# Optimization experiments

Hardware: AMD Instinct MI355X
Metric: run time of the kernel (lower is better)

The kernel has to match this reference:

```python
import jax, jax.numpy as jnp
import numpy as np

HIDDEN = 2048
N_HEADS = 16
HEAD_DIM = HIDDEN // N_HEADS
BATCH = 2
SEQ = 2048
N_CP = max(8, int(HIDDEN * HIDDEN / 128.9))  # 32540 control points


def _spline_to_weight(cp, out_dim, in_dim):
    # Reconstruct full weight matrix by sampling the control-point curve at
    # out_dim*in_dim evenly spaced parameter values (piecewise-linear spline eval).
    n = cp.shape[0]
    t = jnp.linspace(0.0, 1.0, out_dim * in_dim)
    xp = jnp.linspace(0.0, 1.0, n)
    return jnp.interp(t, xp, cp).reshape(out_dim, in_dim)


def setup_inputs() -> dict:
    key = jax.random.key(0)
    ks = jax.random.split(key, 5)
    hidden_states = jax.random.normal(ks[0], (BATCH, SEQ, HIDDEN), dtype=jnp.float32)
    cp_q = jax.random.normal(ks[1], (N_CP,), dtype=jnp.float32) * 0.02
    cp_k = jax.random.normal(ks[2], (N_CP,), dtype=jnp.float32) * 0.02
    cp_v = jax.random.normal(ks[3], (N_CP,), dtype=jnp.float32) * 0.02
    cp_o = jax.random.normal(ks[4], (N_CP,), dtype=jnp.float32) * 0.02
    # additive causal mask [1,1,S,S]
    causal = jnp.tril(jnp.ones((SEQ, SEQ), dtype=bool))
    attention_mask = jnp.where(causal, 0.0, -1e9).astype(jnp.float32)[None, None]
    return {
        'hidden_states': hidden_states,
        'cp_q': cp_q, 'cp_k': cp_k, 'cp_v': cp_v, 'cp_o': cp_o,
        'attention_mask': attention_mask,
    }


def reference(hidden_states, cp_q, cp_k, cp_v, cp_o, attention_mask):
    B, S, H = hidden_states.shape
    q_w = _spline_to_weight(cp_q, H, H)
    k_w = _spline_to_weight(cp_k, H, H)
    v_w = _spline_to_weight(cp_v, H, H)
    o_w = _spline_to_weight(cp_o, H, H)

    # F.linear(x, W) == x @ W.T
    q = (hidden_states @ q_w.T).reshape(B, S, N_HEADS, HEAD_DIM).transpose(0, 2, 1, 3)
    k = (hidden_states @ k_w.T).reshape(B, S, N_HEADS, HEAD_DIM).transpose(0, 2, 1, 3)
    v = (hidden_states @ v_w.T).reshape(B, S, N_HEADS, HEAD_DIM).transpose(0, 2, 1, 3)

    scale = 1.0 / np.sqrt(HEAD_DIM).astype(np.float32)
    scores = jnp.einsum('bhqd,bhkd->bhqk', q, k) * scale + attention_mask
    probs = jax.nn.softmax(scores.astype(jnp.float32), axis=-1).astype(q.dtype)
    attn = jnp.einsum('bhqk,bhkd->bhqd', probs, v)
    attn = attn.transpose(0, 2, 1, 3).reshape(B, S, H)
    return attn @ o_w.T
```

## Files before the change

### kernel.cpp

```cpp
#include <hip/hip_runtime.h>
#include <stdint.h>

typedef unsigned short u16;
typedef __bf16 bf16x8 __attribute__((ext_vector_type(8)));
typedef float f32x4 __attribute__((ext_vector_type(4)));
typedef u16 u16x4 __attribute__((ext_vector_type(4)));

#define MFMA16(a, b, c) __builtin_amdgcn_mfma_f32_16x16x32_bf16((a), (b), (c), 0, 0, 0)

__device__ __forceinline__ u16 f2bf(float f) {
  uint32_t u = __builtin_bit_cast(uint32_t, f);
  u += 0x7FFFu + ((u >> 16) & 1u);
  return (u16)(u >> 16);
}
__device__ __forceinline__ bf16x8 cvt8(f32x4 lo, f32x4 hi) {
  union { u16 u[8]; bf16x8 v; } r;
#pragma unroll
  for (int j = 0; j < 4; j++) { r.u[j] = f2bf(lo[j]); r.u[4 + j] = f2bf(hi[j]); }
  return r.v;
}
__device__ __forceinline__ void gld_lds16(const void* g, void* l) {
  __builtin_amdgcn_global_load_lds(
      (const __attribute__((address_space(1))) uint32_t*)g,
      (__attribute__((address_space(3))) uint32_t*)l, 16, 0, 0);
}

__global__ void prep_kernel(const float* __restrict__ x, const float* __restrict__ cpq,
                            const float* __restrict__ cpk, const float* __restrict__ cpv,
                            const float* __restrict__ cpo, u16* __restrict__ xb,
                            u16* __restrict__ Wqkv, u16* __restrict__ Wo,
                            int n, double factor) {
  int blk = blockIdx.x;
  if (blk < 65536) {
    int idx = blk * 256 + threadIdx.x;
    int w = idx >> 22;
    int i = idx & 4194303;
    const float* cp = (w == 0) ? cpq : (w == 1) ? cpk : (w == 2) ? cpv : cpo;
    double u = (double)i * factor;
    int i0 = (int)u;
    if (i0 > n - 2) i0 = n - 2;
    float fr = (float)(u - (double)i0);
    float f0 = cp[i0], f1 = cp[i0 + 1];
    u16 bv = f2bf(f0 + fr * (f1 - f0));
    if (w < 3) Wqkv[idx] = bv; else Wo[i] = bv;
  } else {
    size_t i = ((size_t)(blk - 65536) * 256 + threadIdx.x) * 8;
    const f32x4* p = (const f32x4*)(x + i);
    *(bf16x8*)(xb + i) = cvt8(p[0], p[1]);
  }
}

__global__ __launch_bounds__(512, 2)
void gemm_qkv(const u16* __restrict__ A, const u16* __restrict__ B,
              u16* __restrict__ oQ, u16* __restrict__ oK, u16* __restrict__ oV) {
  __shared__ __align__(16) u16 As[3 * 128 * 64];
  __shared__ __align__(16) u16 Bs[3 * 256 * 64];
  const int tid = threadIdx.x;
  const int wave = tid >> 6, lane = tid & 63, quad = lane >> 4, l16 = lane & 15;
  const int wm = wave & 1, wn = wave >> 1;

  const int m0 = blockIdx.y * 128, n0 = blockIdx.x * 256;

  size_t aoffg[2], boffg[4];
  int lA[2], lB[4];
#pragma unroll
  for (int u = 0; u < 2; u++) {
    int s = u * 512 + tid, r = s >> 3, c = s & 7, gc = c ^ (r & 7);
    lA[u] = s * 16;
    aoffg[u] = (size_t)(m0 + r) * 4096 + gc * 16;
  }
#pragma unroll
  for (int u = 0; u < 4; u++) {
    int s = u * 512 + tid, r = s >> 3, c = s & 7, gc = c ^ (r & 7);
    lB[u] = s * 16;
    boffg[u] = (size_t)(n0 + r) * 4096 + gc * 16;
  }

  int roA[4], roB[4];
#pragma unroll
  for (int mi = 0; mi < 4; mi++) {
    int row = wm * 64 + mi * 16 + l16;
    roA[mi] = row * 128 + ((quad ^ (row & 7)) * 16);
  }
#pragma unroll
  for (int nj = 0; nj < 4; nj++) {
    int row = wn * 64 + nj * 16 + l16;
    roB[nj] = row * 128 + ((quad ^ (row & 7)) * 16);
  }

  const char* Ab = (const char*)A;
  const char* Bb = (const char*)B;
  char* AsB = (char*)As;
  char* BsB = (char*)Bs;

  f32x4 acc[4][4];
  const f32x4 fz = {0.f, 0.f, 0.f, 0.f};
#pragma unroll
  for (int i = 0; i < 4; i++)
#pragma unroll
    for (int j = 0; j < 4; j++) acc[i][j] = fz;

#define QKV_STAGE(TT, NX)                                                     \
  do {                                                                        \
    size_t kb = (size_t)(TT) * 128;                                           \
    gld_lds16(Ab + aoffg[0] + kb, AsB + (NX) * 16384 + lA[0]);                \
    gld_lds16(Ab + aoffg[1] + kb, AsB + (NX) * 16384 + lA[1]);                \
    gld_lds16(Bb + boffg[0] + kb, BsB + (NX) * 32768 + lB[0]);                \
    gld_lds16(Bb + boffg[1] + kb, BsB + (NX) * 32768 + lB[1]);                \
    gld_lds16(Bb + boffg[2] + kb, BsB + (NX) * 32768 + lB[2]);                \
    gld_lds16(Bb + boffg[3] + kb, BsB + (NX) * 32768 + lB[3]);                \
  } while (0)

#define QKV_BODY(T, CUR, NX, STG, WM)                                         \
  do {                                                                        \
    if (STG) QKV_STAGE((T) + 2, NX);                                          \
    _Pragma("unroll") for (int t = 0; t < 2; t++) {                           \
      bf16x8 af[4], bfv[4];                                                   \
      _Pragma("unroll") for (int mi = 0; mi < 4; mi++)                        \
          af[mi] = *(const bf16x8*)(AsB + (CUR) * 16384 + (roA[mi] ^ (t * 64))); \
      _Pragma("unroll") for (int nj = 0; nj < 4; nj++)                        \
          bfv[nj] = *(const bf16x8*)(BsB + (CUR) * 32768 + (roB[nj] ^ (t * 64))); \
      __builtin_amdgcn_s_setprio(1);                                          \
      _Pragma("unroll") for (int mi = 0; mi < 4; mi++)                        \
          _Pragma("unroll") for (int nj = 0; nj < 4; nj++)                    \
              acc[mi][nj] = MFMA16(af[mi], bfv[nj], acc[mi][nj]);             \
      __builtin_amdgcn_s_setprio(0);                                          \
    }                                                                         \
    if ((WM) == 6) asm volatile("s_waitcnt vmcnt(6)" ::: "memory");           \
    else if ((WM) == 0) asm volatile("s_waitcnt vmcnt(0)" ::: "memory");      \
    if ((WM) >= 0) {                                                          \
      __builtin_amdgcn_s_barrier();                                           \
      __builtin_amdgcn_sched_barrier(0);                                      \
    }                                                                         \
  } while (0)

  QKV_STAGE(0, 0);
  QKV_STAGE(1, 1);
  asm volatile("s_waitcnt vmcnt(6)" ::: "memory");
  __builtin_amdgcn_s_barrier();
  __builtin_amdgcn_sched_barrier(0);

  for (int t = 0; t < 30; t += 3) {
    QKV_BODY(t, 0, 2, true, 6);
    QKV_BODY(t + 1, 1, 0, true, 6);
    QKV_BODY(t + 2, 2, 1, true, 6);
  }
  QKV_BODY(30, 0, 2, false, 0);
  QKV_BODY(31, 1, 0, false, -1);
#undef QKV_BODY
#undef QKV_STAGE

  const float qscale = 0.08838834764831845f;
#pragma unroll
  for (int j = 0; j < 4; j++) {
    int nb = n0 + wn * 64 + j * 16;
    int sel = nb >> 11;
    int h = (nb >> 7) & 15;
    int d = (nb & 127) + l16;
#pragma unroll
    for (int i = 0; i < 4; i++) {
      int mrow = m0 + wm * 64 + i * 16 + quad * 4;
      int bq = mrow >> 11, srow = mrow & 2047;
      if (sel == 2) {
        u16x4 pk = {f2bf(acc[i][j][0]), f2bf(acc[i][j][1]),
                    f2bf(acc[i][j][2]), f2bf(acc[i][j][3])};
        *(u16x4*)&oV[(size_t)(((bq << 4) + h) * 128 + d) * 2048 + srow] = pk;
      } else if (sel == 0) {
        int base = ((bq << 4) + h) * 2048;
#pragma unroll
        for (int r = 0; r < 4; r++)
          oQ[(size_t)(base + srow + r) * 128 + d] = f2bf(acc[i][j][r] * qscale);
      } else {
        int base = ((bq << 4) + h) * 2048;
#pragma unroll
        for (int r = 0; r < 4; r++)
          oK[(size_t)(base + srow + r) * 128 + d] = f2bf(acc[i][j][r]);
      }
    }
  }
}

template <int MODE>
__global__ __launch_bounds__(256, 2)
void gemm_bt(const u16* __restrict__ A, const u16* __restrict__ B,
             u16* __restrict__ oQ, u16* __restrict__ oK, u16* __restrict__ oV,
             float* __restrict__ oC) {
  constexpr int KD = 2048;
  __shared__ __align__(16) u16 As[128 * 64];
  __shared__ __align__(16) u16 Bs[128 * 64];
  const int tid = threadIdx.x;
  const int wave = tid >> 6, lane = tid & 63, quad = lane >> 4, l16 = lane & 15;
  const int wm = wave & 1, wn = wave >> 1;
  const int m0 = blockIdx.y * 128, n0 = blockIdx.x * 128;

  size_t aoff[4], boff[4];
  int lslot[4];
#pragma unroll
  for (int b = 0; b < 4; b++) {
    int s = wave * 256 + b * 64 + lane;
    int r = s >> 3, c = s & 7, gc = c ^ (r & 7);
    lslot[b] = s * 16;
    aoff[b] = (size_t)(m0 + r) * (KD * 2) + gc * 16;
    boff[b] = (size_t)(n0 + r) * (KD * 2) + gc * 16;
  }
  const char* Ab = (const char*)A;
  const char* Bb = (const char*)B;
  char* AsB = (char*)As;
  char* BsB = (char*)Bs;

  f32x4 acc[4][4];
  const f32x4 fz = {0.f, 0.f, 0.f, 0.f};
#pragma unroll
  for (int i = 0; i < 4; i++)
#pragma unroll
    for (int j = 0; j < 4; j++) acc[i][j] = fz;

  for (int kt = 0; kt < KD / 64; ++kt) {
    if (kt) __syncthreads();
#pragma unroll
    for (int b = 0; b < 4; b++) {
      gld_lds16(Ab + aoff[b], AsB + lslot[b]);
      gld_lds16(Bb + boff[b], BsB + lslot[b]);
      aoff[b] += 128;
      boff[b] += 128;
    }
    __syncthreads();
#pragma unroll
    for (int t = 0; t < 2; t++) {
      bf16x8 af[4], bfb[4];
#pragma unroll
      for (int i = 0; i < 4; i++) {
        int row = wm * 64 + i * 16 + l16;
        int ch = (t * 4 + quad) ^ (row & 7);
        af[i] = *(const bf16x8*)(AsB + row * 128 + ch * 16);
      }
#pragma unroll
      for (int j = 0; j < 4; j++) {
        int row = wn * 64 + j * 16 + l16;
        int ch = (t * 4 + quad) ^ (row & 7);
        bfb[j] = *(const bf16x8*)(BsB + row * 128 + ch * 16);
      }
#pragma unroll
      for (int i = 0; i < 4; i++)
#pragma unroll
        for (int j = 0; j < 4; j++) acc[i][j] = MFMA16(af[i], bfb[j], acc[i][j]);
    }
  }

  if (MODE == 0) {
    const float qscale = 0.08838834764831845f;
#pragma unroll
    for (int j = 0; j < 4; j++) {
      int nb = n0 + wn * 64 + j * 16;
      int sel = nb >> 11;
      int h = (nb >> 7) & 15;
      int d = (nb & 127) + l16;
#pragma unroll
      for (int i = 0; i < 4; i++) {
        int mrow = m0 + wm * 64 + i * 16 + quad * 4;
        int bq = mrow >> 11, srow = mrow & 2047;
        if (sel == 2) {
          u16x4 pk = {f2bf(acc[i][j][0]), f2bf(acc[i][j][1]),
                      f2bf(acc[i][j][2]), f2bf(acc[i][j][3])};
          *(u16x4*)&oV[(size_t)(((bq << 4) + h) * 128 + d) * 2048 + srow] = pk;
        } else if (sel == 0) {
          int base = ((bq << 4) + h) * 2048;
#pragma unroll
          for (int r = 0; r < 4; r++)
            oQ[(size_t)(base + srow + r) * 128 + d] = f2bf(acc[i][j][r] * qscale);
        } else {
          int base = ((bq << 4) + h) * 2048;
#pragma unroll
          for (int r = 0; r < 4; r++)
            oK[(size_t)(base + srow + r) * 128 + d] = f2bf(acc[i][j][r]);
        }
      }
    }
  } else {
#pragma unroll
    for (int j = 0; j < 4; j++) {
      int col = n0 + wn * 64 + j * 16 + l16;
#pragma unroll
      for (int i = 0; i < 4; i++) {
        int mrow = m0 + wm * 64 + i * 16 + quad * 4;
#pragma unroll
        for (int r = 0; r < 4; r++) oC[(size_t)(mrow + r) * 2048 + col] = acc[i][j][r];
      }
    }
  }
}

__global__ __launch_bounds__(256, 2)
void flash_attn(const u16* __restrict__ Q, const u16* __restrict__ Kg,
                const u16* __restrict__ Vt, u16* __restrict__ attn) {
  __shared__ __align__(16) u16 Ks[64 * 128];
  __shared__ __align__(16) u16 Vs[128 * 64];
  __shared__ __align__(16) u16 Ps[128 * 72];
  const int tid = threadIdx.x;
  const int wave = tid >> 6, lane = tid & 63, quad = lane >> 4, l16 = lane & 15;
  const int L = blockIdx.x;
  const int bh = L & 31;
  const int qi = (L >> 5) & 7;
  const int qt = (L >= 256) ? (15 - qi) : qi;
  const int q0 = qt * 128;
  const u16* Qb = Q + (size_t)bh * 2048 * 128;
  const u16* Kb = Kg + (size_t)bh * 2048 * 128;
  const u16* Vb = Vt + (size_t)bh * 128 * 2048;

  bf16x8 qf[2][4];
#pragma unroll
  for (int i = 0; i < 2; i++) {
    int row = q0 + wave * 32 + i * 16 + l16;
#pragma unroll
    for (int t = 0; t < 4; t++)
      qf[i][t] = *(const bf16x8*)(Qb + (size_t)row * 128 + t * 32 + quad * 8);
  }

  f32x4 o_acc[2][8];
  const f32x4 fz = {0.f, 0.f, 0.f, 0.f};
#pragma unroll
  for (int i = 0; i < 2; i++)
#pragma unroll
    for (int j = 0; j < 8; j++) o_acc[i][j] = fz;
  float l_i[2] = {0.f, 0.f};

  int koff[4], voff[4], lslot[4];
#pragma unroll
  for (int b = 0; b < 4; b++) {
    int s = wave * 256 + b * 64 + lane;
    lslot[b] = s * 16;
    {
      int r = s >> 4, c = s & 15;
      int gc = (c & 8) | ((c & 7) ^ (r & 7));
      koff[b] = r * 256 + gc * 16;
    }
    {
      int r = s >> 3, c = s & 7;
      int gc = c ^ (r & 7);
      voff[b] = r * 4096 + gc * 16;
    }
  }
  const char* KbB = (const char*)Kb;
  const char* VbB = (const char*)Vb;
  char* KsB = (char*)Ks;
  char* VsB = (char*)Vs;

  const int ktmax = 2 * qt + 1;

  for (int kt = 0; kt <= ktmax; ++kt) {
    const int k0 = kt * 64;
    if (kt) __syncthreads();
#pragma unroll
    for (int b = 0; b < 4; b++) {
      gld_lds16(KbB + (size_t)k0 * 256 + koff[b], KsB + lslot[b]);
      gld_lds16(VbB + (size_t)k0 * 2 + voff[b], VsB + lslot[b]);
    }
    __syncthreads();

    f32x4 st[2][4];
#pragma unroll
    for (int i = 0; i < 2; i++)
#pragma unroll
      for (int j = 0; j < 4; j++) st[i][j] = fz;
#pragma unroll
    for (int j = 0; j < 4; j++) {
      int rowk = j * 16 + l16;
#pragma unroll
      for (int t = 0; t < 4; t++) {
        int cc = t * 4 + quad;
        int ch = (cc & 8) | ((cc & 7) ^ (rowk & 7));
        bf16x8 kfr = *(const bf16x8*)(KsB + rowk * 256 + ch * 16);
        st[0][j] = MFMA16(kfr, qf[0][t], st[0][j]);
        st[1][j] = MFMA16(kfr, qf[1][t], st[1][j]);
      }
    }

    const bool do_mask = (kt >= 2 * qt);
#pragma unroll
    for (int i = 0; i < 2; i++) {
      const int qg = q0 + wave * 32 + i * 16 + l16;
      float lacc = 0.f;
#pragma unroll
      for (int j = 0; j < 4; j++) {
        float p[4];
#pragma unroll
        for (int r = 0; r < 4; r++) {
          float v = st[i][j][r];
          if (do_mask && (k0 + j * 16 + quad * 4 + r > qg)) v = -1e30f;
          p[r] = __expf(v);
        }
        lacc += (p[0] + p[1]) + (p[2] + p[3]);
        u16x4 pk = {f2bf(p[0]), f2bf(p[1]), f2bf(p[2]), f2bf(p[3])};
        *(u16x4*)&Ps[(wave * 32 + i * 16 + l16) * 72 + j * 16 + quad * 4] = pk;
      }
      l_i[i] += lacc;
    }

#pragma unroll
    for (int t = 0; t < 2; t++) {
      bf16x8 af0 = *(const bf16x8*)((char*)Ps + (wave * 32 + l16) * 144 + (t * 32 + quad * 8) * 2);
      bf16x8 af1 = *(const bf16x8*)((char*)Ps + (wave * 32 + 16 + l16) * 144 + (t * 32 + quad * 8) * 2);
#pragma unroll
      for (int j = 0; j < 8; j++) {
        int vrow = j * 16 + l16;
        int ch = (t * 4 + quad) ^ (vrow & 7);
        bf16x8 bfr = *(const bf16x8*)(VsB + vrow * 128 + ch * 16);
        o_acc[0][j] = MFMA16(af0, bfr, o_acc[0][j]);
        o_acc[1][j] = MFMA16(af1, bfr, o_acc[1][j]);
      }
    }
  }

  const int bb = bh >> 4, h = bh & 15;
#pragma unroll
  for (int i = 0; i < 2; i++) {
    float rs = l_i[i];
    rs += __shfl_xor(rs, 16);
    rs += __shfl_xor(rs, 32);
    float inv = 1.f / rs;
#pragma unroll
    for (int r = 0; r < 4; r++) {
      float invr = __shfl(inv, (lane & 48) | (quad * 4 + r), 64);
      int srow = q0 + wave * 32 + i * 16 + quad * 4 + r;
      size_t base = ((size_t)(bb * 2048 + srow)) * 2048 + h * 128;
#pragma unroll
      for (int j = 0; j < 8; j++) attn[base + j * 16 + l16] = f2bf(o_acc[i][j][r] * invr);
    }
  }
}

extern "C" void kernel_launch(void* const* d_in, const int* in_sizes, int n_in,
                              void* d_out, int out_size, void* d_ws, size_t ws_size,
                              hipStream_t stream) {
  (void)n_in; (void)out_size; (void)ws_size;
  const float* x = (const float*)d_in[0];
  const float* cpq = (const float*)d_in[1];
  const float* cpk = (const float*)d_in[2];
  const float* cpv = (const float*)d_in[3];
  const float* cpo = (const float*)d_in[4];
  float* out = (float*)d_out;
  const int ncp = in_sizes[1];
  const double factor = (double)(ncp - 1) / 4194303.0;

  char* ws = (char*)d_ws;
  u16* Wqkv = (u16*)(ws);
  u16* At   = (u16*)(ws);
  u16* Wo = (u16*)(ws + 25165824);
  u16* Qp = (u16*)(ws + 33554432);
  u16* Kp = (u16*)(ws + 50331648);
  u16* Vp = (u16*)(ws + 67108864);
  u16* xb = (u16*)d_out;

  prep_kernel<<<dim3(69632), dim3(256), 0, stream>>>(x, cpq, cpk, cpv, cpo, xb, Wqkv, Wo, ncp, factor);
  gemm_qkv<<<dim3(24, 32), dim3(512), 0, stream>>>(xb, Wqkv, Qp, Kp, Vp);
  flash_attn<<<dim3(512), dim3(256), 0, stream>>>(Qp, Kp, Vp, At);
  gemm_bt<1><<<dim3(16, 32), dim3(256), 0, stream>>>(At, Wo, nullptr, nullptr, nullptr, out);
}
```

Before: 355.6 us.

## Enlarge QKV GEMM tile to 256x384 with double-buffered LDS

The QKV projection GEMM tile grows from 128x256 to 256x384 per block. Each wave now holds an 8x6 accumulator grid, so every LDS fragment is reused more and fewer blocks reload the same global data. The triple-buffered LDS pipeline becomes a double buffer: the next stage is issued only after a barrier that waits for reads of the current buffer to finish. The grid drops from 768 to 256 blocks, which costs occupancy and wave-level parallelism. It also raises register pressure under launch_bounds(512,2), and the LDS use of about 160KB may limit the kernel to one block per CU.

```diff
diff --git a/kernel.cpp b/kernel.cpp
--- a/kernel.cpp
+++ b/kernel.cpp
@@ -53,80 +53,79 @@
 __global__ __launch_bounds__(512, 2)
 void gemm_qkv(const u16* __restrict__ A, const u16* __restrict__ B,
               u16* __restrict__ oQ, u16* __restrict__ oK, u16* __restrict__ oV) {
-  __shared__ __align__(16) u16 As[3 * 128 * 64];
-  __shared__ __align__(16) u16 Bs[3 * 256 * 64];
+  __shared__ __align__(16) u16 As[2 * 256 * 64];
+  __shared__ __align__(16) u16 Bs[2 * 384 * 64];
   const int tid = threadIdx.x;
   const int wave = tid >> 6, lane = tid & 63, quad = lane >> 4, l16 = lane & 15;
   const int wm = wave & 1, wn = wave >> 1;
-
-  const int m0 = blockIdx.y * 128, n0 = blockIdx.x * 256;
-
-  size_t aoffg[2], boffg[4];
-  int lA[2], lB[4];
-#pragma unroll
-  for (int u = 0; u < 2; u++) {
-    int s = u * 512 + tid, r = s >> 3, c = s & 7, gc = c ^ (r & 7);
-    lA[u] = s * 16;
-    aoffg[u] = (size_t)(m0 + r) * 4096 + gc * 16;
-  }
+  const int m0 = blockIdx.y * 256, n0 = blockIdx.x * 384;
+
+  uint32_t aoffg[4], boffg[6];
 #pragma unroll
   for (int u = 0; u < 4; u++) {
     int s = u * 512 + tid, r = s >> 3, c = s & 7, gc = c ^ (r & 7);
-    lB[u] = s * 16;
-    boffg[u] = (size_t)(n0 + r) * 4096 + gc * 16;
-  }
-
-  int roA[4], roB[4];
-#pragma unroll
-  for (int mi = 0; mi < 4; mi++) {
-    int row = wm * 64 + mi * 16 + l16;
-    roA[mi] = row * 128 + ((quad ^ (row & 7)) * 16);
-  }
-#pragma unroll
-  for (int nj = 0; nj < 4; nj++) {
-    int row = wn * 64 + nj * 16 + l16;
-    roB[nj] = row * 128 + ((quad ^ (row & 7)) * 16);
-  }
+    aoffg[u] = (uint32_t)(m0 + r) * 4096u + gc * 16;
+  }
+#pragma unroll
+  for (int u = 0; u < 6; u++) {
+    int s = u * 512 + tid, r = s >> 3, c = s & 7, gc = c ^ (r & 7);
+    boffg[u] = (uint32_t)(n0 + r) * 4096u + gc * 16;
+  }
+
+  const int swz = (quad ^ (l16 & 7)) * 16;
+  const int baseA0 = (wm * 128 + l16) * 128 + swz;
+  const int baseA1 = baseA0 ^ 64;
+  const int baseB0 = (wn * 96 + l16) * 128 + swz;
+  const int baseB1 = baseB0 ^ 64;
 
   const char* Ab = (const char*)A;
   const char* Bb = (const char*)B;
   char* AsB = (char*)As;
   char* BsB = (char*)Bs;
 
-  f32x4 acc[4][4];
+  f32x4 acc[8][6];
   const f32x4 fz = {0.f, 0.f, 0.f, 0.f};
 #pragma unroll
-  for (int i = 0; i < 4; i++)
-#pragma unroll
-    for (int j = 0; j < 4; j++) acc[i][j] = fz;
+  for (int i = 0; i < 8; i++)
+#pragma unroll
+    for (int j = 0; j < 6; j++) acc[i][j] = fz;
 
 #define QKV_STAGE(TT, NX)                                                     \
   do {                                                                        \
-    size_t kb = (size_t)(TT) * 128;                                           \
-    gld_lds16(Ab + aoffg[0] + kb, AsB + (NX) * 16384 + lA[0]);                \
-    gld_lds16(Ab + aoffg[1] + kb, AsB + (NX) * 16384 + lA[1]);                \
-    gld_lds16(Bb + boffg[0] + kb, BsB + (NX) * 32768 + lB[0]);                \
-    gld_lds16(Bb + boffg[1] + kb, BsB + (NX) * 32768 + lB[1]);                \
-    gld_lds16(Bb + boffg[2] + kb, BsB + (NX) * 32768 + lB[2]);                \
-    gld_lds16(Bb + boffg[3] + kb, BsB + (NX) * 32768 + lB[3]);                \
+    uint32_t kb = (uint32_t)(TT) * 128u;                                      \
+    _Pragma("unroll") for (int u = 0; u < 4; u++)                             \
+      gld_lds16(Ab + (size_t)(aoffg[u] + kb),                                 \
+                AsB + (NX) * 32768 + u * 8192 + tid * 16);                    \
+    _Pragma("unroll") for (int u = 0; u < 6; u++)                             \
+      gld_lds16(Bb + (size_t)(boffg[u] + kb),                                 \
+                BsB + (NX) * 49152 + u * 8192 + tid * 16);                    \
   } while (0)
 
-#define QKV_BODY(T, CUR, NX, STG, WM)                                         \
+#define QKV_TSTEP(CUR, BA, BB)                                                \
   do {                                                                        \
-    if (STG) QKV_STAGE((T) + 2, NX);                                          \
-    _Pragma("unroll") for (int t = 0; t < 2; t++) {                           \
-      bf16x8 af[4], bfv[4];                                                   \
-      _Pragma("unroll") for (int mi = 0; mi < 4; mi++)                        \
-          af[mi] = *(const bf16x8*)(AsB + (CUR) * 16384 + (roA[mi] ^ (t * 64))); \
-      _Pragma("unroll") for (int nj = 0; nj < 4; nj++)                        \
-          bfv[nj] = *(const bf16x8*)(BsB + (CUR) * 32768 + (roB[nj] ^ (t * 64))); \
+    bf16x8 bfv[6];                                                            \
+    _Pragma("unroll") for (int j = 0; j < 6; j++)                             \
+      bfv[j] = *(const bf16x8*)(BsB + (CUR) * 49152 + (BB) + j * 2048);       \
+    _Pragma("unroll") for (int i = 0; i < 8; i++) {                           \
+      bf16x8 afv = *(const bf16x8*)(AsB + (CUR) * 32768 + (BA) + i * 2048);   \
       __builtin_amdgcn_s_setprio(1);                                          \
-      _Pragma("unroll") for (int mi = 0; mi < 4; mi++)                        \
-          _Pragma("unroll") for (int nj = 0; nj < 4; nj++)                    \
-              acc[mi][nj] = MFMA16(af[mi], bfv[nj], acc[mi][nj]);             \
+      _Pragma("unroll") for (int j = 0; j < 6; j++)                           \
+        acc[i][j] = MFMA16(afv, bfv[j], acc[i][j]);                           \
       __builtin_amdgcn_s_setprio(0);                                          \
     }                                                                         \
-    if ((WM) == 6) asm volatile("s_waitcnt vmcnt(6)" ::: "memory");           \
+  } while (0)
+
+#define QKV_BODY(T, CUR, STG, WM)                                             \
+  do {                                                                        \
+    QKV_TSTEP(CUR, baseA0, baseB0);                                           \
+    QKV_TSTEP(CUR, baseA1, baseB1);                                           \
+    if (STG) {                                                                \
+      asm volatile("s_waitcnt lgkmcnt(0)" ::: "memory");                      \
+      __builtin_amdgcn_s_barrier();                                           \
+      __builtin_amdgcn_sched_barrier(0);                                      \
+      QKV_STAGE((T) + 2, CUR);                                                \
+    }                                                                         \
+    if ((WM) == 10) asm volatile("s_waitcnt vmcnt(10)" ::: "memory");         \
     else if ((WM) == 0) asm volatile("s_waitcnt vmcnt(0)" ::: "memory");      \
     if ((WM) >= 0) {                                                          \
       __builtin_amdgcn_s_barrier();                                           \
@@ -136,30 +135,30 @@
 
   QKV_STAGE(0, 0);
   QKV_STAGE(1, 1);
-  asm volatile("s_waitcnt vmcnt(6)" ::: "memory");
+  asm volatile("s_waitcnt vmcnt(10)" ::: "memory");
   __builtin_amdgcn_s_barrier();
   __builtin_amdgcn_sched_barrier(0);
 
-  for (int t = 0; t < 30; t += 3) {
-    QKV_BODY(t, 0, 2, true, 6);
-    QKV_BODY(t + 1, 1, 0, true, 6);
-    QKV_BODY(t + 2, 2, 1, true, 6);
-  }
-  QKV_BODY(30, 0, 2, false, 0);
-  QKV_BODY(31, 1, 0, false, -1);
+  for (int t = 0; t < 30; t += 2) {
+    QKV_BODY(t, 0, true, 10);
+    QKV_BODY(t + 1, 1, true, 10);
+  }
+  QKV_BODY(30, 0, false, 0);
+  QKV_BODY(31, 1, false, -1);
 #undef QKV_BODY
+#undef QKV_TSTEP
 #undef QKV_STAGE
 
   const float qscale = 0.08838834764831845f;
 #pragma unroll
-  for (int j = 0; j < 4; j++) {
-    int nb = n0 + wn * 64 + j * 16;
+  for (int j = 0; j < 6; j++) {
+    int nb = n0 + wn * 96 + j * 16;
     int sel = nb >> 11;
     int h = (nb >> 7) & 15;
     int d = (nb & 127) + l16;
 #pragma unroll
-    for (int i = 0; i < 4; i++) {
-      int mrow = m0 + wm * 64 + i * 16 + quad * 4;
+    for (int i = 0; i < 8; i++) {
+      int mrow = m0 + wm * 128 + i * 16 + quad * 4;
       int bq = mrow >> 11, srow = mrow & 2047;
       if (sel == 2) {
         u16x4 pk = {f2bf(acc[i][j][0]), f2bf(acc[i][j][1]),
@@ -452,7 +451,7 @@
   u16* xb = (u16*)d_out;
 
   prep_kernel<<<dim3(69632), dim3(256), 0, stream>>>(x, cpq, cpk, cpv, cpo, xb, Wqkv, Wo, ncp, factor);
-  gemm_qkv<<<dim3(24, 32), dim3(512), 0, stream>>>(xb, Wqkv, Qp, Kp, Vp);
+  gemm_qkv<<<dim3(16, 16), dim3(512), 0, stream>>>(xb, Wqkv, Qp, Kp, Vp);
   flash_attn<<<dim3(512), dim3(256), 0, stream>>>(Qp, Kp, Vp, At);
   gemm_bt<1><<<dim3(16, 32), dim3(256), 0, stream>>>(At, Wo, nullptr, nullptr, nullptr, out);
 }
```

After: 345.4 us. 1.03x faster.
